# Kernel optimization log

Hardware: AMD Instinct MI355X
Metric: run time of the kernel (lower is better)

Reference implementation:

```python
import jax, jax.numpy as jnp
import numpy as np

GRAPH = 50  # top-k neighbors


def setup_inputs() -> dict:
    key = jax.random.key(0)
    k1, k2, k3, k4, k5 = jax.random.split(key, 5)
    B, N, D, C = 2048, 50000, 256, 100
    return {
        "features": jax.random.normal(k1, (B, D), dtype=jnp.float32),
        "anchor_feature": jax.random.normal(k2, (N, D), dtype=jnp.float32),
        "labels": jax.random.randint(k3, (B,), 0, C),
        "t_labels": jax.random.randint(k4, (B,), 0, C),
        "anchor_label": jax.random.randint(k5, (N,), 0, C),
    }


def reference(features, anchor_feature, labels, t_labels, anchor_label):
    # mode == 'knn_sim', reduction=False; t_labels is unpacked but unused.
    # [B, N] dot-product similarity
    sim = jnp.matmul(features, anchor_feature.T)
    # top-k values and indices along anchor dim
    topk_vals, topk_idx = jax.lax.top_k(sim, GRAPH)  # [B, k]
    # label-match mask gathered at the top-k anchors (equivalent to
    # building the full [B, N] eq-mask then torch.gather along dim 1,
    # but gathers anchor labels first to avoid the dense mask)
    nn_labels = anchor_label[topk_idx]               # [B, k]
    mask_k = (labels[:, None] == nn_labels).astype(jnp.float32)
    mean_log_prob_pos = mask_k.sum(axis=1) / GRAPH   # [B]
    mean_sim = topk_vals.sum(axis=1) / GRAPH         # [B]
    # NaN scrub (x != x) -> 0, as in the torch code
    mean_log_prob_pos = jnp.where(jnp.isnan(mean_log_prob_pos), 0.0, mean_log_prob_pos)
    loss = -mean_log_prob_pos                        # [B] (reduction=False)
    return loss, mean_sim
```

## Files before the change

kernel.cpp:

```cpp
#include <hip/hip_runtime.h>
#include <math.h>

#define B_ROWS 2048
#define N_ANCH 50000
#define DIM    256
#define TOPK   50

#define BT 128
#define AT 256
#define KC 32
#define NCHUNK 8
#define NCH 16
#define CHUNK 3125
#define NTILES 13
#define NSAMP 4096
#define CAPG 2048

#define NRB (B_ROWS / BT)
#define TSF (NRB * 8 * 512)
#define TSA (NCH * NTILES * 8 * 1024)

typedef __attribute__((ext_vector_type(8))) short bf16x8;
typedef __attribute__((ext_vector_type(8))) unsigned short u16x8;
typedef __attribute__((ext_vector_type(4))) float f32x4;

#define OFF_B 0
#define OFF_A 16384
#define BUFB  24576
#define SMEM_BYTES (2 * BUFB)

__device__ __forceinline__ void gl_lds16(const void* g, void* l) {
    __builtin_amdgcn_global_load_lds(
        (const __attribute__((address_space(1))) unsigned int*)g,
        (__attribute__((address_space(3))) unsigned int*)l, 16, 0, 0);
}

template<int N>
__device__ __forceinline__ void wait_vmcnt() {
    asm volatile("s_waitcnt vmcnt(%0)" :: "n"(N) : "memory");
}
__device__ __forceinline__ void wait_lgkm0() {
    asm volatile("s_waitcnt lgkmcnt(0)" ::: "memory");
}
__device__ __forceinline__ void pipe_bar() {
    asm volatile("" ::: "memory");
    __builtin_amdgcn_s_barrier();
    asm volatile("" ::: "memory");
}

__device__ __forceinline__ unsigned short f2bf(float x) {
    unsigned u = __float_as_uint(x);
    u += 0x7FFFu + ((u >> 16) & 1u);
    return (unsigned short)(u >> 16);
}

__device__ __forceinline__ unsigned f2ord(float f) {
    unsigned u = __float_as_uint(f);
    return (u & 0x80000000u) ? ~u : (u | 0x80000000u);
}
__device__ __forceinline__ float ord2f(unsigned o) {
    return (o & 0x80000000u) ? __uint_as_float(o & 0x7FFFFFFFu) : __uint_as_float(~o);
}

__device__ __forceinline__ void cvt8(const float4 v0, const float4 v1,
                                     u16x8* H, u16x8* L) {
    float f[8] = {v0.x, v0.y, v0.z, v0.w, v1.x, v1.y, v1.z, v1.w};
    u16x8 h, l;
    #pragma unroll
    for (int j = 0; j < 8; ++j) {
        unsigned short hb = f2bf(f[j]);
        h[j] = hb;
        l[j] = f2bf(f[j] - __uint_as_float((unsigned)hb << 16));
    }
    *H = h; *L = l;
}

__global__ __launch_bounds__(256)
void split_pack_feat(const float* __restrict__ x,
                     unsigned short* __restrict__ hi,
                     unsigned short* __restrict__ lo)
{
    const int S  = blockIdx.x * 256 + threadIdx.x;
    const int s  = S & 511;
    const int c  = (S >> 9) & 7;
    const int rb = S >> 12;
    const int r  = s & 127;
    const int kq = s >> 7;
    const int row = (rb << 7) + r;
    const int k   = (c << 5) + (kq << 3);
    const float4* src = (const float4*)(x + (size_t)row * DIM + k);
    u16x8 H, L;
    cvt8(src[0], src[1], &H, &L);
    *(u16x8*)(hi + (size_t)S * 8) = H;
    *(u16x8*)(lo + (size_t)S * 8) = L;
}

__global__ __launch_bounds__(256)
void split_pack_anc(const float* __restrict__ x,
                    unsigned short* __restrict__ hi,
                    unsigned short* __restrict__ lo)
{
    const int S    = blockIdx.x * 256 + threadIdx.x;
    const int s    = S & 1023;
    const int c    = (S >> 10) & 7;
    const int tg   = S >> 13;
    const int cidx = tg / NTILES;
    const int tile = tg - cidx * NTILES;
    int a = cidx * CHUNK + (tile << 8) + (s & 255);
    if (a >= N_ANCH) a = N_ANCH - 1;
    const int k = (c << 5) + ((s >> 8) << 3);
    const float4* src = (const float4*)(x + (size_t)a * DIM + k);
    u16x8 H, L;
    cvt8(src[0], src[1], &H, &L);
    *(u16x8*)(hi + (size_t)S * 8) = H;
    *(u16x8*)(lo + (size_t)S * 8) = L;
}

#define STAGE_LOADS 3
__device__ __forceinline__ void stage_tile(unsigned char* sb,
                                           const unsigned short* __restrict__ Bsrc,
                                           const unsigned short* __restrict__ Asrc,
                                           int w, int lane)
{
    #pragma unroll
    for (int i = 0; i < 2; ++i) {
        const int t = (w << 1) + i;
        gl_lds16(Bsrc + ((size_t)t << 9) + (lane << 3), sb + OFF_B + (t << 10));
    }
    gl_lds16(Asrc + (((w << 6) + lane) << 3), sb + OFF_A + (w << 10));
}

__device__ __forceinline__ void compute_tile(const unsigned char* sb,
                                             int wm, int wn, int quad, int lx,
                                             f32x4 (&acc)[4][4])
{
    bf16x8 bf[4], af[4];
    #pragma unroll
    for (int tn = 0; tn < 4; ++tn) {
        const int a = (wn << 6) + (tn << 4) + lx;
        bf[tn] = *(const bf16x8*)(sb + OFF_B + (quad << 12) + (a << 4));
    }
    #pragma unroll
    for (int tm = 0; tm < 4; ++tm) {
        const int r = (wm << 6) + (tm << 4) + lx;
        af[tm] = *(const bf16x8*)(sb + OFF_A + (quad << 11) + (r << 4));
    }
    #pragma unroll
    for (int tm = 0; tm < 4; ++tm)
        #pragma unroll
        for (int tn = 0; tn < 4; ++tn)
            acc[tm][tn] = __builtin_amdgcn_mfma_f32_16x16x32_bf16(af[tm], bf[tn], acc[tm][tn], 0, 0, 0);
}

__global__ __launch_bounds__(512, 4)
void knn_sample_gemm(const unsigned short* __restrict__ pfhi,
                     const unsigned short* __restrict__ pflo,
                     const unsigned short* __restrict__ pahi,
                     const unsigned short* __restrict__ palo,
                     float* __restrict__ sims)
{
    __shared__ __align__(16) unsigned char sMem[SMEM_BYTES];

    const int tid  = threadIdx.x;
    const int w    = tid >> 6;
    const int lane = tid & 63;
    const int quad = lane >> 4;
    const int lx   = lane & 15;
    const int wm   = w >> 2;
    const int wn   = w & 3;

    const int id   = blockIdx.x;
    const int xcd  = id & 7;
    const int t    = id >> 3;
    const int rb   = t & 15;
    const int cidx = ((t >> 4) << 3) | xcd;
    const int rbase = rb * BT;
    const int tg    = cidx * NTILES;

    const unsigned short* Fp[3] = {pfhi, pflo, pfhi};
    const unsigned short* Bp[3] = {pahi, pahi, palo};

    auto bsrc = [&](int it) {
        return Bp[it >> 3] + (((size_t)(tg << 3)) + (it & 7)) * 8192;
    };
    auto asrc = [&](int it) {
        return Fp[it >> 3] + (((size_t)(rb << 3)) + (it & 7)) * 4096;
    };

    f32x4 acc[4][4];
    const f32x4 z = {0.f, 0.f, 0.f, 0.f};
    #pragma unroll
    for (int tm = 0; tm < 4; ++tm)
        #pragma unroll
        for (int tn = 0; tn < 4; ++tn) acc[tm][tn] = z;

    stage_tile(sMem, bsrc(0), asrc(0), w, lane);
    __syncthreads();

    int cur = 0;
    for (int it = 0; it < 24; ++it) {
        if (it + 1 < 24) {
            stage_tile(sMem + (cur ^ 1) * BUFB, bsrc(it + 1), asrc(it + 1), w, lane);
            wait_vmcnt<STAGE_LOADS>();
        } else {
            wait_vmcnt<0>();
        }
        pipe_bar();
        compute_tile(sMem + cur * BUFB, wm, wn, quad, lx, acc);
        wait_lgkm0();
        pipe_bar();
        cur ^= 1;
    }

    #pragma unroll
    for (int tm = 0; tm < 4; ++tm)
        #pragma unroll
        for (int tn = 0; tn < 4; ++tn)
            #pragma unroll
            for (int reg = 0; reg < 4; ++reg) {
                int row = rbase + (wm << 6) + (tm << 4) + (quad << 2) + reg;
                int col = (wn << 6) + (tn << 4) + lx;
                sims[(size_t)row * NSAMP + cidx * AT + col] = acc[tm][tn][reg];
            }
}

__global__ __launch_bounds__(256)
void bisect_thresh(const float* __restrict__ sims,
                   uint2* __restrict__ cand, int* __restrict__ cnt,
                   float* __restrict__ Tarr)
{
    __shared__ float sv[NSAMP];
    __shared__ float s_rmin[4], s_rmax[4];
    __shared__ int   s_c, s_ns;

    const int row = blockIdx.x;
    const int tid = threadIdx.x;
    const int lane = tid & 63, w = tid >> 6;
    const unsigned long long below = (lane == 0) ? 0ull : (~0ull >> (64 - lane));

    const float4* S4 = (const float4*)(sims + (size_t)row * NSAMP);
    for (int i = tid; i < NSAMP / 4; i += 256) ((float4*)sv)[i] = S4[i];
    __syncthreads();

    float lmin = INFINITY, lmax = -INFINITY;
    for (int e0 = 0; e0 < NSAMP; e0 += 256) {
        float v = sv[e0 + tid];
        lmin = fminf(lmin, v); lmax = fmaxf(lmax, v);
    }
    #pragma unroll
    for (int off = 32; off; off >>= 1) {
        lmin = fminf(lmin, __shfl_down(lmin, off));
        lmax = fmaxf(lmax, __shfl_down(lmax, off));
    }
    if (lane == 0) { s_rmin[w] = lmin; s_rmax[w] = lmax; }
    __syncthreads();
    float lo = fminf(fminf(s_rmin[0], s_rmin[1]), fminf(s_rmin[2], s_rmin[3]));
    float mx = fmaxf(fmaxf(s_rmax[0], s_rmax[1]), fmaxf(s_rmax[2], s_rmax[3]));
    float hi = ord2f(f2ord(mx) + 1);
    int clo = NSAMP;
    for (int it = 0; it < 32 && clo > 64; ++it) {
        float mid = 0.5f * (lo + hi);
        if (tid == 0) s_c = 0;
        __syncthreads();
        int lc = 0;
        for (int e0 = 0; e0 < NSAMP; e0 += 256) lc += (sv[e0 + tid] >= mid);
        #pragma unroll
        for (int off = 32; off; off >>= 1) lc += __shfl_down(lc, off);
        if (lane == 0) atomicAdd(&s_c, lc);
        __syncthreads();
        int c = s_c;
        if (c >= TOPK) { lo = mid; clo = c; } else hi = mid;
        __syncthreads();
    }
    if (tid == 0) { Tarr[row] = lo; s_ns = 0; }
    __syncthreads();

    for (int e0 = 0; e0 < NSAMP; e0 += 256) {
        int e = e0 + tid;
        float v = sv[e];
        bool pred = (v >= lo);
        unsigned long long mk = __ballot(pred);
        int base = 0;
        if (lane == 0) base = atomicAdd(&s_ns, __popcll(mk));
        base = __shfl(base, 0);
        if (pred) {
            int ofs = base + __popcll(mk & below);
            int anchor = (e >> 8) * CHUNK + (e & 255);
            cand[(size_t)row * CAPG + ofs] = make_uint2(__float_as_uint(v), (unsigned)anchor);
        }
    }
    __syncthreads();
    if (tid == 0) cnt[row] = s_ns;
}

__global__ __launch_bounds__(512, 4)
void knn_mfma_append(const unsigned short* __restrict__ pfhi,
                     const unsigned short* __restrict__ pflo,
                     const unsigned short* __restrict__ pahi,
                     const unsigned short* __restrict__ palo,
                     const float* __restrict__ Tarr,
                     uint2* __restrict__ cand, int* __restrict__ cnt)
{
    __shared__ __align__(16) unsigned char sMem[SMEM_BYTES];
    __shared__ float s_T[BT];

    const int tid  = threadIdx.x;
    const int w    = tid >> 6;
    const int lane = tid & 63;
    const int quad = lane >> 4;
    const int lx   = lane & 15;
    const int wm   = w >> 2;
    const int wn   = w & 3;

    const int id   = blockIdx.x;
    const int xcd  = id & 7;
    const int t    = id >> 3;
    const int rb   = t & 15;
    const int gseq = t >> 4;
    const int g    = (gseq << 3) | xcd;
    const int cidx = g & 15;
    const int tile = 1 + (g >> 4);
    const int rbase = rb * BT;

    if (tid < BT) s_T[tid] = Tarr[rbase + tid];

    const unsigned short* Fp[3] = {pfhi, pflo, pfhi};
    const unsigned short* Bp[3] = {pahi, pahi, palo};

    auto bsrc = [&](int it) {
        return Bp[it >> 3] + (((size_t)((cidx * NTILES + tile) << 3)) + (it & 7)) * 8192;
    };
    auto asrc = [&](int it) {
        return Fp[it >> 3] + (((size_t)(rb << 3)) + (it & 7)) * 4096;
    };

    stage_tile(sMem, bsrc(0), asrc(0), w, lane);
    __syncthreads();

    float thr[4][4];
    #pragma unroll
    for (int tm = 0; tm < 4; ++tm)
        #pragma unroll
        for (int reg = 0; reg < 4; ++reg)
            thr[tm][reg] = s_T[(wm << 6) + (tm << 4) + (quad << 2) + reg];

    f32x4 acc[4][4];
    const f32x4 z = {0.f, 0.f, 0.f, 0.f};
    #pragma unroll
    for (int tm = 0; tm < 4; ++tm)
        #pragma unroll
        for (int tn = 0; tn < 4; ++tn) acc[tm][tn] = z;

    int cur = 0;
    for (int it = 0; it < 24; ++it) {
        if (it + 1 < 24) {
            stage_tile(sMem + (cur ^ 1) * BUFB, bsrc(it + 1), asrc(it + 1), w, lane);
            wait_vmcnt<STAGE_LOADS>();
        } else {
            wait_vmcnt<0>();
        }
        pipe_bar();
        compute_tile(sMem + cur * BUFB, wm, wn, quad, lx, acc);
        wait_lgkm0();
        pipe_bar();
        cur ^= 1;
    }

    const int abase = cidx * CHUNK + tile * AT;
    const int valid = min(AT, CHUNK - tile * AT);

    #pragma unroll
    for (int tm = 0; tm < 4; ++tm)
        #pragma unroll
        for (int tn = 0; tn < 4; ++tn)
            #pragma unroll
            for (int reg = 0; reg < 4; ++reg) {
                const float v    = acc[tm][tn][reg];
                const int   aoff = (wn << 6) + (tn << 4) + lx;
                if (aoff < valid && v >= thr[tm][reg]) {
                    const int row = rbase + (wm << 6) + (tm << 4) + (quad << 2) + reg;
                    int slot = atomicAdd(&cnt[row], 1);
                    if (slot < CAPG)
                        cand[(size_t)row * CAPG + slot] =
                            make_uint2(__float_as_uint(v), (unsigned)(abase + aoff));
                }
            }
}

__global__ __launch_bounds__(256)
void knn_final(const uint2* __restrict__ cand, const int* __restrict__ cnt,
               const int* __restrict__ labels, const int* __restrict__ anchor_label,
               float* __restrict__ out)
{
    __shared__ float pv[CAPG];
    __shared__ int   pi[CAPG];
    __shared__ float fv[128];
    __shared__ int   fi[128];
    __shared__ float s_rmin[4], s_rmax[4];
    __shared__ int   s_c, s_m, s_cm;
    __shared__ float s_sum;

    const int row = blockIdx.x;
    const int tid = threadIdx.x;
    const int lane = tid & 63, w = tid >> 6;
    const unsigned long long below = (lane == 0) ? 0ull : (~0ull >> (64 - lane));

    if (tid == 0) { s_sum = 0.f; s_cm = 0; }

    int ns = cnt[row]; if (ns > CAPG) ns = CAPG;
    for (int e0 = 0; e0 < ns; e0 += 256) {
        int e = e0 + tid;
        if (e < ns) {
            uint2 c = cand[(size_t)row * CAPG + e];
            pv[e] = __uint_as_float(c.x); pi[e] = (int)c.y;
        }
    }
    __syncthreads();
    const int mylab = labels[row];

    float lmin = INFINITY, lmax = -INFINITY;
    for (int e0 = 0; e0 < ns; e0 += 256) {
        int e = e0 + tid;
        if (e < ns) { float v = pv[e]; lmin = fminf(lmin, v); lmax = fmaxf(lmax, v); }
    }
    #pragma unroll
    for (int off = 32; off; off >>= 1) {
        lmin = fminf(lmin, __shfl_down(lmin, off));
        lmax = fmaxf(lmax, __shfl_down(lmax, off));
    }
    if (lane == 0) { s_rmin[w] = lmin; s_rmax[w] = lmax; }
    __syncthreads();
    float lo = fminf(fminf(s_rmin[0], s_rmin[1]), fminf(s_rmin[2], s_rmin[3]));
    float mx = fmaxf(fmaxf(s_rmax[0], s_rmax[1]), fmaxf(s_rmax[2], s_rmax[3]));
    float hi = ord2f(f2ord(mx) + 1);
    int clo = ns;
    for (int it = 0; it < 32 && clo > 96; ++it) {
        float mid = 0.5f * (lo + hi);
        if (tid == 0) s_c = 0;
        __syncthreads();
        int lc = 0;
        for (int e0 = 0; e0 < ns; e0 += 256) {
            int e = e0 + tid;
            lc += (e < ns && pv[e] >= mid);
        }
        #pragma unroll
        for (int off = 32; off; off >>= 1) lc += __shfl_down(lc, off);
        if (lane == 0) atomicAdd(&s_c, lc);
        __syncthreads();
        int c = s_c;
        if (c >= TOPK) { lo = mid; clo = c; } else hi = mid;
        __syncthreads();
    }

    if (clo <= 96) {
        if (tid == 0) s_m = 0;
        __syncthreads();
        for (int e0 = 0; e0 < ns; e0 += 256) {
            int e = e0 + tid;
            bool pred = (e < ns) && (pv[e] >= lo);
            unsigned long long mk = __ballot(pred);
            int base = 0;
            if (lane == 0) base = atomicAdd(&s_m, __popcll(mk));
            base = __shfl(base, 0);
            if (pred) {
                int ofs = base + __popcll(mk & below);
                fv[ofs] = pv[e]; fi[ofs] = pi[e];
            }
        }
        __syncthreads();
        const int m = s_m;
        if (tid < m) {
            float v = fv[tid]; int id = fi[tid];
            int r = 0;
            for (int q = 0; q < m; ++q) {
                float vq = fv[q];
                r += (vq > v) || (vq == v && fi[q] < id);
            }
            if (r < TOPK) {
                atomicAdd(&s_sum, v);
                if (anchor_label[id] == mylab) atomicAdd(&s_cm, 1);
            }
        }
    } else {
        for (int e0 = 0; e0 < ns; e0 += 256) {
            int e = e0 + tid;
            if (e < ns) {
                float v = pv[e]; int id = pi[e];
                int r = 0;
                for (int q = 0; q < ns; ++q) {
                    float vq = pv[q];
                    r += (vq > v) || (vq == v && pi[q] < id);
                }
                if (r < TOPK) {
                    atomicAdd(&s_sum, v);
                    if (anchor_label[id] == mylab) atomicAdd(&s_cm, 1);
                }
            }
        }
    }
    __syncthreads();
    if (tid == 0) {
        float mlp = (float)s_cm / (float)TOPK;
        out[row]          = -mlp;
        out[B_ROWS + row] = s_sum / (float)TOPK;
    }
}

extern "C" void kernel_launch(void* const* d_in, const int* in_sizes, int n_in,
                              void* d_out, int out_size, void* d_ws, size_t ws_size,
                              hipStream_t stream)
{
    const float* feat         = (const float*)d_in[0];
    const float* anc          = (const float*)d_in[1];
    const int*   labels       = (const int*)d_in[2];
    const int*   anchor_label = (const int*)d_in[4];
    float* out = (float*)d_out;

    char* ws = (char*)d_ws;
    size_t off = 0;
    unsigned short* pfhi = (unsigned short*)(ws + off); off += (size_t)TSF * 16;
    unsigned short* pflo = (unsigned short*)(ws + off); off += (size_t)TSF * 16;
    unsigned short* pahi = (unsigned short*)(ws + off); off += (size_t)TSA * 16;
    unsigned short* palo = (unsigned short*)(ws + off); off += (size_t)TSA * 16;
    float* sims = (float*)(ws + off);        off += (size_t)B_ROWS * NSAMP * 4;
    uint2* cand = (uint2*)sims;
    int*   cnt  = (int*)(ws + off);          off += (size_t)B_ROWS * 4;
    float* Tarr = (float*)(ws + off);        off += (size_t)B_ROWS * 4;

    hipLaunchKernelGGL(split_pack_feat, dim3(TSF / 256), dim3(256), 0, stream,
                       feat, pfhi, pflo);
    hipLaunchKernelGGL(split_pack_anc, dim3(TSA / 256), dim3(256), 0, stream,
                       anc, pahi, palo);
    hipLaunchKernelGGL(knn_sample_gemm, dim3(256), dim3(512), 0, stream,
                       pfhi, pflo, pahi, palo, sims);
    hipLaunchKernelGGL(bisect_thresh, dim3(B_ROWS), dim3(256), 0, stream,
                       sims, cand, cnt, Tarr);
    hipLaunchKernelGGL(knn_mfma_append, dim3(3072), dim3(512), 0, stream,
                       pfhi, pflo, pahi, palo, Tarr, cand, cnt);
    hipLaunchKernelGGL(knn_final, dim3(B_ROWS), dim3(256), 0, stream,
                       cand, cnt, labels, anchor_label, out);
}
```

Before: 534.0 us.

## Enlarge append GEMM row tile to 256 with 1024-thread blocks

```diff
diff --git a/kernel.cpp b/kernel.cpp
--- a/kernel.cpp
+++ b/kernel.cpp
@@ -6,7 +6,8 @@
 #define DIM    256
 #define TOPK   50
 
-#define BT 128
+#define BTS 128
+#define BTL 256
 #define AT 256
 #define KC 32
 #define NCHUNK 8
@@ -16,18 +17,18 @@
 #define NSAMP 4096
 #define CAPG 2048
 
-#define NRB (B_ROWS / BT)
-#define TSF (NRB * 8 * 512)
-#define TSA (NCH * NTILES * 8 * 1024)
+#define TSF  (16 * 8 * 512)
+#define TSF2 (8 * 8 * 1024)
+#define TSA  (NCH * NTILES * 8 * 1024)
 
 typedef __attribute__((ext_vector_type(8))) short bf16x8;
 typedef __attribute__((ext_vector_type(8))) unsigned short u16x8;
 typedef __attribute__((ext_vector_type(4))) float f32x4;
 
-#define OFF_B 0
-#define OFF_A 16384
-#define BUFB  24576
-#define SMEM_BYTES (2 * BUFB)
+#define OFF_A_S 16384
+#define BUFB_S  24576
+#define OFF_A_L 16384
+#define BUFB_L  32768
 
 __device__ __forceinline__ void gl_lds16(const void* g, void* l) {
     __builtin_amdgcn_global_load_lds(
@@ -87,6 +88,26 @@
     const int r  = s & 127;
     const int kq = s >> 7;
     const int row = (rb << 7) + r;
+    const int k   = (c << 5) + (kq << 3);
+    const float4* src = (const float4*)(x + (size_t)row * DIM + k);
+    u16x8 H, L;
+    cvt8(src[0], src[1], &H, &L);
+    *(u16x8*)(hi + (size_t)S * 8) = H;
+    *(u16x8*)(lo + (size_t)S * 8) = L;
+}
+
+__global__ __launch_bounds__(256)
+void split_pack_feat256(const float* __restrict__ x,
+                        unsigned short* __restrict__ hi,
+                        unsigned short* __restrict__ lo)
+{
+    const int S  = blockIdx.x * 256 + threadIdx.x;
+    const int s  = S & 1023;
+    const int c  = (S >> 10) & 7;
+    const int rb = S >> 13;
+    const int r  = s & 255;
+    const int kq = s >> 8;
+    const int row = (rb << 8) + r;
     const int k   = (c << 5) + (kq << 3);
     const float4* src = (const float4*)(x + (size_t)row * DIM + k);
     u16x8 H, L;
@@ -116,34 +137,35 @@
     *(u16x8*)(lo + (size_t)S * 8) = L;
 }
 
-#define STAGE_LOADS 3
-__device__ __forceinline__ void stage_tile(unsigned char* sb,
-                                           const unsigned short* __restrict__ Bsrc,
-                                           const unsigned short* __restrict__ Asrc,
-                                           int w, int lane)
+
+#define STAGE_LOADS_S 3
+__device__ __forceinline__ void stage_tile_s(unsigned char* sb,
+                                             const unsigned short* __restrict__ Bsrc,
+                                             const unsigned short* __restrict__ Asrc,
+                                             int w, int lane)
 {
     #pragma unroll
     for (int i = 0; i < 2; ++i) {
         const int t = (w << 1) + i;
-        gl_lds16(Bsrc + ((size_t)t << 9) + (lane << 3), sb + OFF_B + (t << 10));
-    }
-    gl_lds16(Asrc + (((w << 6) + lane) << 3), sb + OFF_A + (w << 10));
-}
-
-__device__ __forceinline__ void compute_tile(const unsigned char* sb,
-                                             int wm, int wn, int quad, int lx,
-                                             f32x4 (&acc)[4][4])
+        gl_lds16(Bsrc + ((size_t)t << 9) + (lane << 3), sb + (t << 10));
+    }
+    gl_lds16(Asrc + (((w << 6) + lane) << 3), sb + OFF_A_S + (w << 10));
+}
+
+__device__ __forceinline__ void compute_tile_s(const unsigned char* sb,
+                                               int wm, int wn, int quad, int lx,
+                                               f32x4 (&acc)[4][4])
 {
     bf16x8 bf[4], af[4];
     #pragma unroll
     for (int tn = 0; tn < 4; ++tn) {
         const int a = (wn << 6) + (tn << 4) + lx;
-        bf[tn] = *(const bf16x8*)(sb + OFF_B + (quad << 12) + (a << 4));
+        bf[tn] = *(const bf16x8*)(sb + (quad << 12) + (a << 4));
     }
     #pragma unroll
     for (int tm = 0; tm < 4; ++tm) {
         const int r = (wm << 6) + (tm << 4) + lx;
-        af[tm] = *(const bf16x8*)(sb + OFF_A + (quad << 11) + (r << 4));
+        af[tm] = *(const bf16x8*)(sb + OFF_A_S + (quad << 11) + (r << 4));
     }
     #pragma unroll
     for (int tm = 0; tm < 4; ++tm)
@@ -159,7 +181,7 @@
                      const unsigned short* __restrict__ palo,
                      float* __restrict__ sims)
 {
-    __shared__ __align__(16) unsigned char sMem[SMEM_BYTES];
+    __shared__ __align__(16) unsigned char sMem[2 * BUFB_S];
 
     const int tid  = threadIdx.x;
     const int w    = tid >> 6;
@@ -174,7 +196,7 @@
     const int t    = id >> 3;
     const int rb   = t & 15;
     const int cidx = ((t >> 4) << 3) | xcd;
-    const int rbase = rb * BT;
+    const int rbase = rb * BTS;
     const int tg    = cidx * NTILES;
 
     const unsigned short* Fp[3] = {pfhi, pflo, pfhi};
@@ -194,19 +216,19 @@
         #pragma unroll
         for (int tn = 0; tn < 4; ++tn) acc[tm][tn] = z;
 
-    stage_tile(sMem, bsrc(0), asrc(0), w, lane);
+    stage_tile_s(sMem, bsrc(0), asrc(0), w, lane);
     __syncthreads();
 
     int cur = 0;
     for (int it = 0; it < 24; ++it) {
         if (it + 1 < 24) {
-            stage_tile(sMem + (cur ^ 1) * BUFB, bsrc(it + 1), asrc(it + 1), w, lane);
-            wait_vmcnt<STAGE_LOADS>();
+            stage_tile_s(sMem + (cur ^ 1) * BUFB_S, bsrc(it + 1), asrc(it + 1), w, lane);
+            wait_vmcnt<STAGE_LOADS_S>();
         } else {
             wait_vmcnt<0>();
         }
         pipe_bar();
-        compute_tile(sMem + cur * BUFB, wm, wn, quad, lx, acc);
+        compute_tile_s(sMem + cur * BUFB_S, wm, wn, quad, lx, acc);
         wait_lgkm0();
         pipe_bar();
         cur ^= 1;
@@ -293,16 +315,49 @@
     if (tid == 0) cnt[row] = s_ns;
 }
 
-__global__ __launch_bounds__(512, 4)
-void knn_mfma_append(const unsigned short* __restrict__ pfhi,
-                     const unsigned short* __restrict__ pflo,
+
+#define STAGE_LOADS_L 2
+__device__ __forceinline__ void stage_tile_l(unsigned char* sb,
+                                             const unsigned short* __restrict__ Bsrc,
+                                             const unsigned short* __restrict__ Asrc,
+                                             int w, int lane)
+{
+    gl_lds16(Bsrc + ((size_t)w << 9) + (lane << 3), sb + (w << 10));
+    gl_lds16(Asrc + ((size_t)w << 9) + (lane << 3), sb + OFF_A_L + (w << 10));
+}
+
+__device__ __forceinline__ void compute_tile_l(const unsigned char* sb,
+                                               int wm, int wn, int quad, int lx,
+                                               f32x4 (&acc)[4][4])
+{
+    bf16x8 bf[4], af[4];
+    #pragma unroll
+    for (int tn = 0; tn < 4; ++tn) {
+        const int a = (wn << 6) + (tn << 4) + lx;
+        bf[tn] = *(const bf16x8*)(sb + (quad << 12) + (a << 4));
+    }
+    #pragma unroll
+    for (int tm = 0; tm < 4; ++tm) {
+        const int r = (wm << 6) + (tm << 4) + lx;
+        af[tm] = *(const bf16x8*)(sb + OFF_A_L + (quad << 12) + (r << 4));
+    }
+    #pragma unroll
+    for (int tm = 0; tm < 4; ++tm)
+        #pragma unroll
+        for (int tn = 0; tn < 4; ++tn)
+            acc[tm][tn] = __builtin_amdgcn_mfma_f32_16x16x32_bf16(af[tm], bf[tn], acc[tm][tn], 0, 0, 0);
+}
+
+__global__ __launch_bounds__(1024, 4)
+void knn_mfma_append(const unsigned short* __restrict__ qfhi,
+                     const unsigned short* __restrict__ qflo,
                      const unsigned short* __restrict__ pahi,
                      const unsigned short* __restrict__ palo,
                      const float* __restrict__ Tarr,
                      uint2* __restrict__ cand, int* __restrict__ cnt)
 {
-    __shared__ __align__(16) unsigned char sMem[SMEM_BYTES];
-    __shared__ float s_T[BT];
+    __shared__ __align__(16) unsigned char sMem[2 * BUFB_L];
+    __shared__ float s_T[BTL];
 
     const int tid  = threadIdx.x;
     const int w    = tid >> 6;
@@ -315,26 +370,26 @@
     const int id   = blockIdx.x;
     const int xcd  = id & 7;
     const int t    = id >> 3;
-    const int rb   = t & 15;
-    const int gseq = t >> 4;
+    const int rb   = t & 7;
+    const int gseq = t >> 3;
     const int g    = (gseq << 3) | xcd;
     const int cidx = g & 15;
     const int tile = 1 + (g >> 4);
-    const int rbase = rb * BT;
-
-    if (tid < BT) s_T[tid] = Tarr[rbase + tid];
-
-    const unsigned short* Fp[3] = {pfhi, pflo, pfhi};
+    const int rbase = rb * BTL;
+
+    if (tid < BTL) s_T[tid] = Tarr[rbase + tid];
+
+    const unsigned short* Fp[3] = {qfhi, qflo, qfhi};
     const unsigned short* Bp[3] = {pahi, pahi, palo};
 
     auto bsrc = [&](int it) {
         return Bp[it >> 3] + (((size_t)((cidx * NTILES + tile) << 3)) + (it & 7)) * 8192;
     };
     auto asrc = [&](int it) {
-        return Fp[it >> 3] + (((size_t)(rb << 3)) + (it & 7)) * 4096;
+        return Fp[it >> 3] + (((size_t)(rb << 3)) + (it & 7)) * 8192;
     };
 
-    stage_tile(sMem, bsrc(0), asrc(0), w, lane);
+    stage_tile_l(sMem, bsrc(0), asrc(0), w, lane);
     __syncthreads();
 
     float thr[4][4];
@@ -354,13 +409,13 @@
     int cur = 0;
     for (int it = 0; it < 24; ++it) {
         if (it + 1 < 24) {
-            stage_tile(sMem + (cur ^ 1) * BUFB, bsrc(it + 1), asrc(it + 1), w, lane);
-            wait_vmcnt<STAGE_LOADS>();
+            stage_tile_l(sMem + (cur ^ 1) * BUFB_L, bsrc(it + 1), asrc(it + 1), w, lane);
+            wait_vmcnt<STAGE_LOADS_L>();
         } else {
             wait_vmcnt<0>();
         }
         pipe_bar();
-        compute_tile(sMem + cur * BUFB, wm, wn, quad, lx, acc);
+        compute_tile_l(sMem + cur * BUFB_L, wm, wn, quad, lx, acc);
         wait_lgkm0();
         pipe_bar();
         cur ^= 1;
@@ -520,6 +575,8 @@
     size_t off = 0;
     unsigned short* pfhi = (unsigned short*)(ws + off); off += (size_t)TSF * 16;
     unsigned short* pflo = (unsigned short*)(ws + off); off += (size_t)TSF * 16;
+    unsigned short* qfhi = (unsigned short*)(ws + off); off += (size_t)TSF2 * 16;
+    unsigned short* qflo = (unsigned short*)(ws + off); off += (size_t)TSF2 * 16;
     unsigned short* pahi = (unsigned short*)(ws + off); off += (size_t)TSA * 16;
     unsigned short* palo = (unsigned short*)(ws + off); off += (size_t)TSA * 16;
     float* sims = (float*)(ws + off);        off += (size_t)B_ROWS * NSAMP * 4;
@@ -529,14 +586,16 @@
 
     hipLaunchKernelGGL(split_pack_feat, dim3(TSF / 256), dim3(256), 0, stream,
                        feat, pfhi, pflo);
+    hipLaunchKernelGGL(split_pack_feat256, dim3(TSF2 / 256), dim3(256), 0, stream,
+                       feat, qfhi, qflo);
     hipLaunchKernelGGL(split_pack_anc, dim3(TSA / 256), dim3(256), 0, stream,
                        anc, pahi, palo);
     hipLaunchKernelGGL(knn_sample_gemm, dim3(256), dim3(512), 0, stream,
                        pfhi, pflo, pahi, palo, sims);
     hipLaunchKernelGGL(bisect_thresh, dim3(B_ROWS), dim3(256), 0, stream,
                        sims, cand, cnt, Tarr);
-    hipLaunchKernelGGL(knn_mfma_append, dim3(3072), dim3(512), 0, stream,
-                       pfhi, pflo, pahi, palo, Tarr, cand, cnt);
+    hipLaunchKernelGGL(knn_mfma_append, dim3(1536), dim3(1024), 0, stream,
+                       qfhi, qflo, pahi, palo, Tarr, cand, cnt);
     hipLaunchKernelGGL(knn_final, dim3(B_ROWS), dim3(256), 0, stream,
                        cand, cnt, labels, anchor_label, out);
 }
```

After: 558.0 us. 4.5% more time.

## Triple-buffer GEMM LDS staging with one barrier per step and MFMA priority

Applied to the files above, without the earlier changes.

```diff
diff --git a/kernel.cpp b/kernel.cpp
--- a/kernel.cpp
+++ b/kernel.cpp
@@ -27,7 +27,7 @@
 #define OFF_B 0
 #define OFF_A 16384
 #define BUFB  24576
-#define SMEM_BYTES (2 * BUFB)
+#define SMEM_BYTES (3 * BUFB)
 
 __device__ __forceinline__ void gl_lds16(const void* g, void* l) {
     __builtin_amdgcn_global_load_lds(
@@ -145,12 +145,15 @@
         const int r = (wm << 6) + (tm << 4) + lx;
         af[tm] = *(const bf16x8*)(sb + OFF_A + (quad << 11) + (r << 4));
     }
+    __builtin_amdgcn_s_setprio(1);
     #pragma unroll
     for (int tm = 0; tm < 4; ++tm)
         #pragma unroll
         for (int tn = 0; tn < 4; ++tn)
             acc[tm][tn] = __builtin_amdgcn_mfma_f32_16x16x32_bf16(af[tm], bf[tn], acc[tm][tn], 0, 0, 0);
-}
+    __builtin_amdgcn_s_setprio(0);
+}
+
 
 __global__ __launch_bounds__(512, 4)
 void knn_sample_gemm(const unsigned short* __restrict__ pfhi,
@@ -194,22 +197,18 @@
         #pragma unroll
         for (int tn = 0; tn < 4; ++tn) acc[tm][tn] = z;
 
-    stage_tile(sMem, bsrc(0), asrc(0), w, lane);
-    __syncthreads();
-
-    int cur = 0;
+    stage_tile(sMem + 0 * BUFB, bsrc(0), asrc(0), w, lane);
+    stage_tile(sMem + 1 * BUFB, bsrc(1), asrc(1), w, lane);
+    __syncthreads();
+
     for (int it = 0; it < 24; ++it) {
-        if (it + 1 < 24) {
-            stage_tile(sMem + (cur ^ 1) * BUFB, bsrc(it + 1), asrc(it + 1), w, lane);
-            wait_vmcnt<STAGE_LOADS>();
-        } else {
-            wait_vmcnt<0>();
-        }
+        if (it + 2 < 24)
+            stage_tile(sMem + ((it + 2) % 3) * BUFB, bsrc(it + 2), asrc(it + 2), w, lane);
+        compute_tile(sMem + (it % 3) * BUFB, wm, wn, quad, lx, acc);
+        wait_lgkm0();
+        if (it + 2 < 24)      wait_vmcnt<STAGE_LOADS>();
+        else if (it + 1 < 24) wait_vmcnt<0>();
         pipe_bar();
-        compute_tile(sMem + cur * BUFB, wm, wn, quad, lx, acc);
-        wait_lgkm0();
-        pipe_bar();
-        cur ^= 1;
     }
 
     #pragma unroll
@@ -334,7 +333,8 @@
         return Fp[it >> 3] + (((size_t)(rb << 3)) + (it & 7)) * 4096;
     };
 
-    stage_tile(sMem, bsrc(0), asrc(0), w, lane);
+    stage_tile(sMem + 0 * BUFB, bsrc(0), asrc(0), w, lane);
+    stage_tile(sMem + 1 * BUFB, bsrc(1), asrc(1), w, lane);
     __syncthreads();
 
     float thr[4][4];
@@ -351,19 +351,14 @@
         #pragma unroll
         for (int tn = 0; tn < 4; ++tn) acc[tm][tn] = z;
 
-    int cur = 0;
     for (int it = 0; it < 24; ++it) {
-        if (it + 1 < 24) {
-            stage_tile(sMem + (cur ^ 1) * BUFB, bsrc(it + 1), asrc(it + 1), w, lane);
-            wait_vmcnt<STAGE_LOADS>();
-        } else {
-            wait_vmcnt<0>();
-        }
+        if (it + 2 < 24)
+            stage_tile(sMem + ((it + 2) % 3) * BUFB, bsrc(it + 2), asrc(it + 2), w, lane);
+        compute_tile(sMem + (it % 3) * BUFB, wm, wn, quad, lx, acc);
+        wait_lgkm0();
+        if (it + 2 < 24)      wait_vmcnt<STAGE_LOADS>();
+        else if (it + 1 < 24) wait_vmcnt<0>();
         pipe_bar();
-        compute_tile(sMem + cur * BUFB, wm, wn, quad, lx, acc);
-        wait_lgkm0();
-        pipe_bar();
-        cur ^= 1;
     }
 
     const int abase = cidx * CHUNK + tile * AT;
```

Measured after the change: 526.7 us. Within noise of the previous version (-1.4%).

## Use single bf16 pass with error-bounded candidate margin and exact rescoring

Applied to the files above, without the earlier changes.

```diff
diff --git a/kernel.cpp b/kernel.cpp
--- a/kernel.cpp
+++ b/kernel.cpp
@@ -15,6 +15,7 @@
 #define NTILES 13
 #define NSAMP 4096
 #define CAPG 2048
+#define RESC 512
 
 #define NRB (B_ROWS / BT)
 #define TSF (NRB * 8 * 512)
@@ -27,7 +28,8 @@
 #define OFF_B 0
 #define OFF_A 16384
 #define BUFB  24576
-#define SMEM_BYTES (2 * BUFB)
+#define SMEM_S (3 * BUFB)
+#define SMEM_L (2 * BUFB)
 
 __device__ __forceinline__ void gl_lds16(const void* g, void* l) {
     __builtin_amdgcn_global_load_lds(
@@ -62,23 +64,36 @@
     return (o & 0x80000000u) ? __uint_as_float(o & 0x7FFFFFFFu) : __uint_as_float(~o);
 }
 
-__device__ __forceinline__ void cvt8(const float4 v0, const float4 v1,
-                                     u16x8* H, u16x8* L) {
+__device__ __forceinline__ float eps_from(const float* eb) {
+    return 0.0079f * sqrtf(eb[0] * eb[1]) + 0.05f;
+}
+
+__global__ __launch_bounds__(256)
+void rownorm_max(const float* __restrict__ x, int nrows, unsigned* __restrict__ outbits)
+{
+    const int lane = threadIdx.x & 63;
+    const int row  = blockIdx.x * 4 + (threadIdx.x >> 6);
+    float s = 0.f;
+    if (row < nrows) {
+        float4 v = ((const float4*)(x + (size_t)row * DIM))[lane];
+        s = v.x * v.x + v.y * v.y + v.z * v.z + v.w * v.w;
+    }
+    #pragma unroll
+    for (int off = 32; off; off >>= 1) s += __shfl_down(s, off);
+    if (lane == 0 && row < nrows)
+        atomicMax(outbits, __float_as_uint(s));
+}
+
+__device__ __forceinline__ u16x8 cvt8h(const float4 v0, const float4 v1) {
     float f[8] = {v0.x, v0.y, v0.z, v0.w, v1.x, v1.y, v1.z, v1.w};
-    u16x8 h, l;
-    #pragma unroll
-    for (int j = 0; j < 8; ++j) {
-        unsigned short hb = f2bf(f[j]);
-        h[j] = hb;
-        l[j] = f2bf(f[j] - __uint_as_float((unsigned)hb << 16));
-    }
-    *H = h; *L = l;
+    u16x8 h;
+    #pragma unroll
+    for (int j = 0; j < 8; ++j) h[j] = f2bf(f[j]);
+    return h;
 }
 
 __global__ __launch_bounds__(256)
-void split_pack_feat(const float* __restrict__ x,
-                     unsigned short* __restrict__ hi,
-                     unsigned short* __restrict__ lo)
+void split_pack_feat(const float* __restrict__ x, unsigned short* __restrict__ hi)
 {
     const int S  = blockIdx.x * 256 + threadIdx.x;
     const int s  = S & 511;
@@ -89,16 +104,11 @@
     const int row = (rb << 7) + r;
     const int k   = (c << 5) + (kq << 3);
     const float4* src = (const float4*)(x + (size_t)row * DIM + k);
-    u16x8 H, L;
-    cvt8(src[0], src[1], &H, &L);
-    *(u16x8*)(hi + (size_t)S * 8) = H;
-    *(u16x8*)(lo + (size_t)S * 8) = L;
+    *(u16x8*)(hi + (size_t)S * 8) = cvt8h(src[0], src[1]);
 }
 
 __global__ __launch_bounds__(256)
-void split_pack_anc(const float* __restrict__ x,
-                    unsigned short* __restrict__ hi,
-                    unsigned short* __restrict__ lo)
+void split_pack_anc(const float* __restrict__ x, unsigned short* __restrict__ hi)
 {
     const int S    = blockIdx.x * 256 + threadIdx.x;
     const int s    = S & 1023;
@@ -110,10 +120,7 @@
     if (a >= N_ANCH) a = N_ANCH - 1;
     const int k = (c << 5) + ((s >> 8) << 3);
     const float4* src = (const float4*)(x + (size_t)a * DIM + k);
-    u16x8 H, L;
-    cvt8(src[0], src[1], &H, &L);
-    *(u16x8*)(hi + (size_t)S * 8) = H;
-    *(u16x8*)(lo + (size_t)S * 8) = L;
+    *(u16x8*)(hi + (size_t)S * 8) = cvt8h(src[0], src[1]);
 }
 
 #define STAGE_LOADS 3
@@ -145,21 +152,21 @@
         const int r = (wm << 6) + (tm << 4) + lx;
         af[tm] = *(const bf16x8*)(sb + OFF_A + (quad << 11) + (r << 4));
     }
+    __builtin_amdgcn_s_setprio(1);
     #pragma unroll
     for (int tm = 0; tm < 4; ++tm)
         #pragma unroll
         for (int tn = 0; tn < 4; ++tn)
             acc[tm][tn] = __builtin_amdgcn_mfma_f32_16x16x32_bf16(af[tm], bf[tn], acc[tm][tn], 0, 0, 0);
+    __builtin_amdgcn_s_setprio(0);
 }
 
 __global__ __launch_bounds__(512, 4)
 void knn_sample_gemm(const unsigned short* __restrict__ pfhi,
-                     const unsigned short* __restrict__ pflo,
                      const unsigned short* __restrict__ pahi,
-                     const unsigned short* __restrict__ palo,
                      float* __restrict__ sims)
 {
-    __shared__ __align__(16) unsigned char sMem[SMEM_BYTES];
+    __shared__ __align__(16) unsigned char sMem[SMEM_S];
 
     const int tid  = threadIdx.x;
     const int w    = tid >> 6;
@@ -177,15 +184,8 @@
     const int rbase = rb * BT;
     const int tg    = cidx * NTILES;
 
-    const unsigned short* Fp[3] = {pfhi, pflo, pfhi};
-    const unsigned short* Bp[3] = {pahi, pahi, palo};
-
-    auto bsrc = [&](int it) {
-        return Bp[it >> 3] + (((size_t)(tg << 3)) + (it & 7)) * 8192;
-    };
-    auto asrc = [&](int it) {
-        return Fp[it >> 3] + (((size_t)(rb << 3)) + (it & 7)) * 4096;
-    };
+    auto bsrc = [&](int c) { return pahi + (((size_t)(tg << 3)) + c) * 8192; };
+    auto asrc = [&](int c) { return pfhi + (((size_t)(rb << 3)) + c) * 4096; };
 
     f32x4 acc[4][4];
     const f32x4 z = {0.f, 0.f, 0.f, 0.f};
@@ -194,22 +194,18 @@
         #pragma unroll
         for (int tn = 0; tn < 4; ++tn) acc[tm][tn] = z;
 
-    stage_tile(sMem, bsrc(0), asrc(0), w, lane);
-    __syncthreads();
-
-    int cur = 0;
-    for (int it = 0; it < 24; ++it) {
-        if (it + 1 < 24) {
-            stage_tile(sMem + (cur ^ 1) * BUFB, bsrc(it + 1), asrc(it + 1), w, lane);
-            wait_vmcnt<STAGE_LOADS>();
-        } else {
-            wait_vmcnt<0>();
-        }
+    stage_tile(sMem + 0 * BUFB, bsrc(0), asrc(0), w, lane);
+    stage_tile(sMem + 1 * BUFB, bsrc(1), asrc(1), w, lane);
+    __syncthreads();
+
+    for (int it = 0; it < NCHUNK; ++it) {
+        if (it + 2 < NCHUNK)
+            stage_tile(sMem + ((it + 2) % 3) * BUFB, bsrc(it + 2), asrc(it + 2), w, lane);
+        compute_tile(sMem + (it % 3) * BUFB, wm, wn, quad, lx, acc);
+        wait_lgkm0();
+        if (it + 2 < NCHUNK)      wait_vmcnt<STAGE_LOADS>();
+        else if (it + 1 < NCHUNK) wait_vmcnt<0>();
         pipe_bar();
-        compute_tile(sMem + cur * BUFB, wm, wn, quad, lx, acc);
-        wait_lgkm0();
-        pipe_bar();
-        cur ^= 1;
     }
 
     #pragma unroll
@@ -227,7 +223,7 @@
 __global__ __launch_bounds__(256)
 void bisect_thresh(const float* __restrict__ sims,
                    uint2* __restrict__ cand, int* __restrict__ cnt,
-                   float* __restrict__ Tarr)
+                   float* __restrict__ Tarr, const float* __restrict__ epsf)
 {
     __shared__ float sv[NSAMP];
     __shared__ float s_rmin[4], s_rmax[4];
@@ -237,6 +233,7 @@
     const int tid = threadIdx.x;
     const int lane = tid & 63, w = tid >> 6;
     const unsigned long long below = (lane == 0) ? 0ull : (~0ull >> (64 - lane));
+    const float eps2 = 2.f * eps_from(epsf);
 
     const float4* S4 = (const float4*)(sims + (size_t)row * NSAMP);
     for (int i = tid; i < NSAMP / 4; i += 256) ((float4*)sv)[i] = S4[i];
@@ -275,10 +272,11 @@
     if (tid == 0) { Tarr[row] = lo; s_ns = 0; }
     __syncthreads();
 
+    const float cut = lo - eps2;
     for (int e0 = 0; e0 < NSAMP; e0 += 256) {
         int e = e0 + tid;
         float v = sv[e];
-        bool pred = (v >= lo);
+        bool pred = (v >= cut);
         unsigned long long mk = __ballot(pred);
         int base = 0;
         if (lane == 0) base = atomicAdd(&s_ns, __popcll(mk));
@@ -286,7 +284,8 @@
         if (pred) {
             int ofs = base + __popcll(mk & below);
             int anchor = (e >> 8) * CHUNK + (e & 255);
-            cand[(size_t)row * CAPG + ofs] = make_uint2(__float_as_uint(v), (unsigned)anchor);
+            if (ofs < CAPG)
+                cand[(size_t)row * CAPG + ofs] = make_uint2(__float_as_uint(v), (unsigned)anchor);
         }
     }
     __syncthreads();
@@ -295,13 +294,11 @@
 
 __global__ __launch_bounds__(512, 4)
 void knn_mfma_append(const unsigned short* __restrict__ pfhi,
-                     const unsigned short* __restrict__ pflo,
                      const unsigned short* __restrict__ pahi,
-                     const unsigned short* __restrict__ palo,
-                     const float* __restrict__ Tarr,
+                     const float* __restrict__ Tarr, const float* __restrict__ epsf,
                      uint2* __restrict__ cand, int* __restrict__ cnt)
 {
-    __shared__ __align__(16) unsigned char sMem[SMEM_BYTES];
+    __shared__ __align__(16) unsigned char sMem[SMEM_L];
     __shared__ float s_T[BT];
 
     const int tid  = threadIdx.x;
@@ -321,18 +318,14 @@
     const int cidx = g & 15;
     const int tile = 1 + (g >> 4);
     const int rbase = rb * BT;
+    const float eps2 = 2.f * eps_from(epsf);
 
     if (tid < BT) s_T[tid] = Tarr[rbase + tid];
 
-    const unsigned short* Fp[3] = {pfhi, pflo, pfhi};
-    const unsigned short* Bp[3] = {pahi, pahi, palo};
-
-    auto bsrc = [&](int it) {
-        return Bp[it >> 3] + (((size_t)((cidx * NTILES + tile) << 3)) + (it & 7)) * 8192;
+    auto bsrc = [&](int c) {
+        return pahi + (((size_t)((cidx * NTILES + tile) << 3)) + c) * 8192;
     };
-    auto asrc = [&](int it) {
-        return Fp[it >> 3] + (((size_t)(rb << 3)) + (it & 7)) * 4096;
-    };
+    auto asrc = [&](int c) { return pfhi + (((size_t)(rb << 3)) + c) * 4096; };
 
     stage_tile(sMem, bsrc(0), asrc(0), w, lane);
     __syncthreads();
@@ -342,7 +335,7 @@
     for (int tm = 0; tm < 4; ++tm)
         #pragma unroll
         for (int reg = 0; reg < 4; ++reg)
-            thr[tm][reg] = s_T[(wm << 6) + (tm << 4) + (quad << 2) + reg];
+            thr[tm][reg] = s_T[(wm << 6) + (tm << 4) + (quad << 2) + reg] - eps2;
 
     f32x4 acc[4][4];
     const f32x4 z = {0.f, 0.f, 0.f, 0.f};
@@ -352,9 +345,9 @@
         for (int tn = 0; tn < 4; ++tn) acc[tm][tn] = z;
 
     int cur = 0;
-    for (int it = 0; it < 24; ++it) {
-        if (it + 1 < 24) {
-            stage_tile(sMem + (cur ^ 1) * BUFB, bsrc(it + 1), asrc(it + 1), w, lane);
+    for (int c = 0; c < NCHUNK; ++c) {
+        if (c + 1 < NCHUNK) {
+            stage_tile(sMem + (cur ^ 1) * BUFB, bsrc(c + 1), asrc(c + 1), w, lane);
             wait_vmcnt<STAGE_LOADS>();
         } else {
             wait_vmcnt<0>();
@@ -387,15 +380,38 @@
             }
 }
 
+__device__ __forceinline__ float coop_dot3(const float4 f4,
+                                           const float* __restrict__ anc,
+                                           int id, int lane)
+{
+    float4 a4 = ((const float4*)(anc + (size_t)id * DIM))[lane];
+    float av[4] = {a4.x, a4.y, a4.z, a4.w};
+    float fw[4] = {f4.x, f4.y, f4.z, f4.w};
+    float s = 0.f;
+    #pragma unroll
+    for (int e = 0; e < 4; ++e) {
+        float a = av[e], f = fw[e];
+        float ah = __uint_as_float((unsigned)f2bf(a) << 16);
+        float al = __uint_as_float((unsigned)f2bf(a - ah) << 16);
+        float fh = __uint_as_float((unsigned)f2bf(f) << 16);
+        float fl = __uint_as_float((unsigned)f2bf(f - fh) << 16);
+        s += ah * fh + al * fh + ah * fl;
+    }
+    #pragma unroll
+    for (int off = 32; off; off >>= 1) s += __shfl_down(s, off);
+    return s;
+}
+
 __global__ __launch_bounds__(256)
 void knn_final(const uint2* __restrict__ cand, const int* __restrict__ cnt,
                const int* __restrict__ labels, const int* __restrict__ anchor_label,
-               float* __restrict__ out)
+               const float* __restrict__ feat, const float* __restrict__ anc,
+               const float* __restrict__ epsf, float* __restrict__ out)
 {
     __shared__ float pv[CAPG];
     __shared__ int   pi[CAPG];
-    __shared__ float fv[128];
-    __shared__ int   fi[128];
+    __shared__ float fv[RESC];
+    __shared__ int   fi[RESC];
     __shared__ float s_rmin[4], s_rmax[4];
     __shared__ int   s_c, s_m, s_cm;
     __shared__ float s_sum;
@@ -404,8 +420,11 @@
     const int tid = threadIdx.x;
     const int lane = tid & 63, w = tid >> 6;
     const unsigned long long below = (lane == 0) ? 0ull : (~0ull >> (64 - lane));
+    const float eps2 = 2.f * eps_from(epsf);
 
     if (tid == 0) { s_sum = 0.f; s_cm = 0; }
+
+    const float4 f4 = ((const float4*)(feat + (size_t)row * DIM))[lane];
 
     int ns = cnt[row]; if (ns > CAPG) ns = CAPG;
     for (int e0 = 0; e0 < ns; e0 += 256) {
@@ -434,7 +453,7 @@
     float mx = fmaxf(fmaxf(s_rmax[0], s_rmax[1]), fmaxf(s_rmax[2], s_rmax[3]));
     float hi = ord2f(f2ord(mx) + 1);
     int clo = ns;
-    for (int it = 0; it < 32 && clo > 96; ++it) {
+    for (int it = 0; it < 32 && clo > 64; ++it) {
         float mid = 0.5f * (lo + hi);
         if (tid == 0) s_c = 0;
         __syncthreads();
@@ -452,48 +471,60 @@
         __syncthreads();
     }
 
-    if (clo <= 96) {
-        if (tid == 0) s_m = 0;
-        __syncthreads();
-        for (int e0 = 0; e0 < ns; e0 += 256) {
-            int e = e0 + tid;
-            bool pred = (e < ns) && (pv[e] >= lo);
-            unsigned long long mk = __ballot(pred);
-            int base = 0;
-            if (lane == 0) base = atomicAdd(&s_m, __popcll(mk));
-            base = __shfl(base, 0);
-            if (pred) {
-                int ofs = base + __popcll(mk & below);
-                fv[ofs] = pv[e]; fi[ofs] = pi[e];
-            }
-        }
-        __syncthreads();
-        const int m = s_m;
-        if (tid < m) {
-            float v = fv[tid]; int id = fi[tid];
+    if (tid == 0) s_m = 0;
+    __syncthreads();
+    const float cut = lo - eps2;
+    for (int e0 = 0; e0 < ns; e0 += 256) {
+        int e = e0 + tid;
+        bool pred = (e < ns) && (pv[e] >= cut);
+        unsigned long long mk = __ballot(pred);
+        int base = 0;
+        if (lane == 0) base = atomicAdd(&s_m, __popcll(mk));
+        base = __shfl(base, 0);
+        if (pred) {
+            int ofs = base + __popcll(mk & below);
+            if (ofs < RESC) { fv[ofs] = pv[e]; fi[ofs] = pi[e]; }
+        }
+    }
+    __syncthreads();
+    const int m = s_m;
+
+    if (clo <= 64 && m <= RESC) {
+        for (int j = w; j < m; j += 4) {
+            float v = coop_dot3(f4, anc, fi[j], lane);
+            if (lane == 0) fv[j] = v;
+        }
+        __syncthreads();
+        for (int e = tid; e < m; e += 256) {
+            float v = fv[e]; int idx = fi[e];
             int r = 0;
             for (int q = 0; q < m; ++q) {
                 float vq = fv[q];
-                r += (vq > v) || (vq == v && fi[q] < id);
+                r += (vq > v) || (vq == v && fi[q] < idx);
             }
             if (r < TOPK) {
                 atomicAdd(&s_sum, v);
-                if (anchor_label[id] == mylab) atomicAdd(&s_cm, 1);
+                if (anchor_label[idx] == mylab) atomicAdd(&s_cm, 1);
             }
         }
     } else {
+        for (int j = w; j < ns; j += 4) {
+            float v = coop_dot3(f4, anc, pi[j], lane);
+            if (lane == 0) pv[j] = v;
+        }
+        __syncthreads();
         for (int e0 = 0; e0 < ns; e0 += 256) {
             int e = e0 + tid;
             if (e < ns) {
-                float v = pv[e]; int id = pi[e];
+                float v = pv[e]; int idx = pi[e];
                 int r = 0;
                 for (int q = 0; q < ns; ++q) {
                     float vq = pv[q];
-                    r += (vq > v) || (vq == v && pi[q] < id);
+                    r += (vq > v) || (vq == v && pi[q] < idx);
                 }
                 if (r < TOPK) {
                     atomicAdd(&s_sum, v);
-                    if (anchor_label[id] == mylab) atomicAdd(&s_cm, 1);
+                    if (anchor_label[idx] == mylab) atomicAdd(&s_cm, 1);
                 }
             }
         }
@@ -519,24 +550,29 @@
     char* ws = (char*)d_ws;
     size_t off = 0;
     unsigned short* pfhi = (unsigned short*)(ws + off); off += (size_t)TSF * 16;
-    unsigned short* pflo = (unsigned short*)(ws + off); off += (size_t)TSF * 16;
     unsigned short* pahi = (unsigned short*)(ws + off); off += (size_t)TSA * 16;
-    unsigned short* palo = (unsigned short*)(ws + off); off += (size_t)TSA * 16;
     float* sims = (float*)(ws + off);        off += (size_t)B_ROWS * NSAMP * 4;
     uint2* cand = (uint2*)sims;
     int*   cnt  = (int*)(ws + off);          off += (size_t)B_ROWS * 4;
     float* Tarr = (float*)(ws + off);        off += (size_t)B_ROWS * 4;
-
+    float* epsf = (float*)(ws + off);        off += 8;
+    unsigned* epsb = (unsigned*)epsf;
+
+    hipMemsetAsync(epsf, 0, 8, stream);
+    hipLaunchKernelGGL(rownorm_max, dim3(B_ROWS / 4), dim3(256), 0, stream,
+                       feat, B_ROWS, epsb + 0);
+    hipLaunchKernelGGL(rownorm_max, dim3(N_ANCH / 4), dim3(256), 0, stream,
+                       anc, N_ANCH, epsb + 1);
     hipLaunchKernelGGL(split_pack_feat, dim3(TSF / 256), dim3(256), 0, stream,
-                       feat, pfhi, pflo);
+                       feat, pfhi);
     hipLaunchKernelGGL(split_pack_anc, dim3(TSA / 256), dim3(256), 0, stream,
-                       anc, pahi, palo);
+                       anc, pahi);
     hipLaunchKernelGGL(knn_sample_gemm, dim3(256), dim3(512), 0, stream,
-                       pfhi, pflo, pahi, palo, sims);
+                       pfhi, pahi, sims);
     hipLaunchKernelGGL(bisect_thresh, dim3(B_ROWS), dim3(256), 0, stream,
-                       sims, cand, cnt, Tarr);
+                       sims, cand, cnt, Tarr, epsf);
     hipLaunchKernelGGL(knn_mfma_append, dim3(3072), dim3(512), 0, stream,
-                       pfhi, pflo, pahi, palo, Tarr, cand, cnt);
+                       pfhi, pahi, Tarr, epsf, cand, cnt);
     hipLaunchKernelGGL(knn_final, dim3(B_ROWS), dim3(256), 0, stream,
-                       cand, cnt, labels, anchor_label, out);
-}
+                       cand, cnt, labels, anchor_label, feat, anc, epsf, out);
+}
```

New measurement: 1.284 ms. +140.4%, slower.
